# Kernel tuning notes

Hardware: AMD Instinct MI355X
Metric: run time of the kernel (lower is better)

Reference implementation:

```python
import jax, jax.numpy as jnp
import numpy as np


def _compute_gradient(f, src, dst, egw):
    # f: [b, c, n] node features; src/dst: [b, e] edge endpoints; egw: [b, e, d]
    # gradient at node src = sum_edges pinvdx * (f[dst] - f[src])
    fT = f.transpose(0, 2, 1)  # b, n, c
    n = fT.shape[1]
    f_dst = jnp.take_along_axis(fT, dst[..., None], axis=1)  # b, e, c
    f_src = jnp.take_along_axis(fT, src[..., None], axis=1)  # b, e, c
    msg = egw[..., :, None] * (f_dst - f_src)[..., None, :]  # b, e, d, c
    b, e, d, c = msg.shape

    def seg(m, s):
        return jax.ops.segment_sum(m.reshape(e, d * c), s, num_segments=n)

    grad = jax.vmap(seg)(msg, src)  # b, n, d*c
    return grad.transpose(0, 2, 1)  # b, d*c, n


def _forward(x, t, nodes, node_weights, edge_gradient_weights, modes, sp_L,
             fc0_w, fc0_b, Wc, Ws, W0, ws_w, ws_b, gws_w, gws_b,
             fc1_w, fc1_b, fc2_w, fc2_b, directed_edges):
    D = nodes.shape[-1]
    # Fourier bases: modes [k,d,w] scaled by sp_L [d,w]
    temp = jnp.einsum('bxd,kdw->bxkw', nodes, modes * sp_L)
    bc, bs = jnp.cos(temp), jnp.sin(temp)
    b0 = jnp.ones(temp[:, :, :1, :].shape, temp.dtype)
    nw = node_weights[:, :, None, :]
    wbc, wbs, wb0 = bc * nw, bs * nw, b0 * nw

    x_value = x[:, :, :D]
    h = jnp.concatenate([x, t], -1) @ fc0_w + fc0_b  # b, n, c
    h = h.transpose(0, 2, 1)  # b, c, n

    src = directed_edges[..., 0]
    dst = directed_edges[..., 1]
    nlayers = ws_w.shape[0]
    for i in range(nlayers):
        # spectral convolution (real Fourier transform on scattered points)
        xc = jnp.einsum('bcx,bxkw->bckw', h, wbc)
        xs = -jnp.einsum('bcx,bxkw->bckw', h, wbs)
        x0 = jnp.einsum('bcx,bxkw->bckw', h, wb0)
        fc_ = jnp.einsum('bikw,iokw->bokw', xc, Wc[i]) - jnp.einsum('bikw,iokw->bokw', xs, Ws[i])
        fs_ = jnp.einsum('bikw,iokw->bokw', xs, Wc[i]) + jnp.einsum('bikw,iokw->bokw', xc, Ws[i])
        f0_ = jnp.einsum('bikw,iokw->bokw', x0, W0[i])
        x1 = (jnp.einsum('bokw,bxkw->box', f0_, b0)
              + 2.0 * jnp.einsum('bokw,bxkw->box', fc_, bc)
              - 2.0 * jnp.einsum('bokw,bxkw->box', fs_, bs))
        # pointwise linear (Conv1d kernel size 1)
        x2 = jnp.einsum('oc,bcx->box', ws_w[i], h) + ws_b[i][None, :, None]
        # gradient operator + softsign + Conv1d
        g = _compute_gradient(h, src, dst, edge_gradient_weights)  # b, d*c, n
        g = g / (1.0 + jnp.abs(g))  # softsign
        x3 = jnp.einsum('oc,bcx->box', gws_w[i], g) + gws_b[i][None, :, None]
        h = x1 + x2 + x3
        if i != nlayers - 1:
            h = jax.nn.gelu(h, approximate=False)

    h = h.transpose(0, 2, 1)  # b, n, c
    h = jax.nn.gelu(h @ fc1_w + fc1_b, approximate=False)
    h = h @ fc2_w + fc2_b
    return x_value + t * h


def setup_inputs() -> dict:
    B, N, E = 2, 20000, 100000
    D, W, K, C, L, FC, OUT = 3, 1, 128, 128, 3, 128, 3
    key = jax.random.key(0)
    k = jax.random.split(key, 16)
    x = jax.random.normal(k[0], (B, N, D), jnp.float32)
    t = jax.random.uniform(k[1], (B, N, 1), jnp.float32)
    node_mask = jnp.ones((B, N, 1), jnp.int32)
    nodes = jax.random.uniform(k[2], (B, N, D), jnp.float32)
    node_weights = jax.random.uniform(k[3], (B, N, W), jnp.float32) / N
    directed_edges = jax.random.randint(k[4], (B, E, 2), 0, N)
    edge_gradient_weights = jax.random.normal(k[5], (B, E, D), jnp.float32)
    modes = jax.random.normal(k[6], (K, D, W), jnp.float32) * (2.0 * np.pi)
    sp_L = jnp.ones((D, W), jnp.float32)
    fc0_w = jax.random.normal(k[7], (D + 1, C), jnp.float32) * 0.1
    fc0_b = jnp.zeros((C,), jnp.float32)
    scale = 1.0 / (C * C)
    Wc = jax.random.uniform(k[8], (L, C, C, K, W), jnp.float32) * scale
    Ws = jax.random.uniform(k[9], (L, C, C, K, W), jnp.float32) * scale
    W0 = jax.random.uniform(k[10], (L, C, C, 1, W), jnp.float32) * scale
    ws_w = jax.random.normal(k[11], (L, C, C), jnp.float32) * 0.05
    ws_b = jnp.zeros((L, C), jnp.float32)
    gws_w = jax.random.normal(k[12], (L, C, D * C), jnp.float32) * 0.05
    gws_b = jnp.zeros((L, C), jnp.float32)
    fc1_w = jax.random.normal(k[13], (C, FC), jnp.float32) * 0.05
    fc1_b = jnp.zeros((FC,), jnp.float32)
    fc2_w = jax.random.normal(k[14], (FC, OUT), jnp.float32) * 0.05
    fc2_b = jnp.zeros((OUT,), jnp.float32)
    return dict(x=x, t=t, node_mask=node_mask, nodes=nodes, node_weights=node_weights,
                directed_edges=directed_edges, edge_gradient_weights=edge_gradient_weights,
                modes=modes, sp_L=sp_L, fc0_w=fc0_w, fc0_b=fc0_b, Wc=Wc, Ws=Ws, W0=W0,
                ws_w=ws_w, ws_b=ws_b, gws_w=gws_w, gws_b=gws_b,
                fc1_w=fc1_w, fc1_b=fc1_b, fc2_w=fc2_w, fc2_b=fc2_b)


def reference(x, t, node_mask, nodes, node_weights, directed_edges, edge_gradient_weights,
              modes, sp_L, fc0_w, fc0_b, Wc, Ws, W0, ws_w, ws_b, gws_w, gws_b,
              fc1_w, fc1_b, fc2_w, fc2_b):
    del node_mask  # unpacked but unused in the original forward
    return _forward(x, t, nodes, node_weights, edge_gradient_weights, modes, sp_L,
                    fc0_w, fc0_b, Wc, Ws, W0, ws_w, ws_b, gws_w, gws_b,
                    fc1_w, fc1_b, fc2_w, fc2_b, directed_edges)
```

## Files before the change

### kernel.cpp

```cpp
#include <hip/hip_runtime.h>
#include <math.h>

#define BB 2
#define NN 20000
#define EE 100000
#define DD 3
#define KK 128
#define CC 128
#define LL 3
#define FCC 128
#define GJ (DD*CC)
#define KR 768
#define NP 20096
#define NCHK 157
#define G1CH 79
#define G1N 256

typedef __attribute__((ext_vector_type(8))) short bf16x8;
typedef __attribute__((ext_vector_type(4))) float f32x4;

__device__ inline unsigned short f2bf(float f) {
  unsigned int u = __float_as_uint(f);
  u += 0x7fffu + ((u >> 16) & 1u);
  return (unsigned short)(u >> 16);
}
__device__ inline float bf2f(unsigned short u) {
  return __uint_as_float(((unsigned int)u) << 16);
}

__device__ float d_nw[BB*NN];
__device__ __align__(16) unsigned short d_stackT[(size_t)BB*NP*KR];
__device__ __align__(16) unsigned short d_bcT[(size_t)BB*KK*NP];
__device__ __align__(16) unsigned short d_bsT[(size_t)BB*KK*NP];
__device__ __align__(16) unsigned short d_hTwT[(size_t)BB*CC*NP];
__device__ __align__(16) float d_hnewT[(size_t)BB*NP*CC];
__device__ __align__(16) float d_uT[(size_t)BB*NP*FCC];
__device__ __align__(16) unsigned short d_Amatb[BB*CC*KR];
__device__ __align__(16) unsigned short d_fc1wb[FCC*CC];
__device__ __align__(16) float d_part[(size_t)BB*G1CH*2*128*128];
__device__ float d_xc[BB*CC*KK];
__device__ float d_xs[BB*CC*KK];
__device__ float d_x0p[BB*NCHK*CC];
__device__ float d_fcv[BB*CC*KK];
__device__ float d_fsv[BB*CC*KK];
__device__ float d_bias[BB*CC];
__device__ int d_cnt[BB*NN];
__device__ int d_cursor[BB*NN];
__device__ int d_off[BB*(NN+1)];
__device__ __align__(16) float4 d_erec[(size_t)BB*EE];

__global__ __launch_bounds__(128) void k_basis(const float* __restrict__ nodes,
                                               const float* __restrict__ nodew,
                                               const float* __restrict__ modes,
                                               const float* __restrict__ spL) {
  int bn = blockIdx.x;
  int k  = threadIdx.x;
  int b = bn / NN, n = bn % NN;
  float x0 = nodes[bn*3+0], x1 = nodes[bn*3+1], x2 = nodes[bn*3+2];
  float tmp = x0*modes[k*3+0]*spL[0] + x1*modes[k*3+1]*spL[1] + x2*modes[k*3+2]*spL[2];
  float cv = cosf(tmp), sv = sinf(tmp);
  size_t row = (size_t)(b*NP + n);
  d_stackT[row*KR + k]       = f2bf(cv);
  d_stackT[row*KR + 128 + k] = f2bf(sv);
  if (k == 0) d_nw[bn] = nodew[bn];
}

__global__ __launch_bounds__(256) void k_basisT() {
  __shared__ unsigned short t1[32][136];
  __shared__ unsigned short t2[32][136];
  int blk = blockIdx.x;
  int nt = blk % 628, b = blk / 628;
  int n0 = nt*32;
  int tid = threadIdx.x;
  int kl = tid & 127, ng = tid >> 7;
  for (int nn = ng; nn < 32; nn += 2) {
    int n = n0 + nn;
    unsigned short cv = 0, sv = 0;
    if (n < NN) {
      const unsigned short* sp = d_stackT + ((size_t)(b*NP + n))*KR;
      cv = sp[kl]; sv = sp[128 + kl];
    }
    t1[nn][kl] = cv;
    t2[nn][kl] = sv;
  }
  __syncthreads();
  int nl = tid & 31, kg = tid >> 5;
  for (int k = kg; k < 128; k += 8) {
    d_bcT[((size_t)(b*KK + k))*NP + n0 + nl] = t1[nl][k];
    d_bsT[((size_t)(b*KK + k))*NP + n0 + nl] = t2[nl][k];
  }
}

__global__ __launch_bounds__(256) void k_csr_zero() {
  int tid = blockIdx.x*256 + threadIdx.x;
  if (tid < BB*NN) { d_cnt[tid] = 0; d_cursor[tid] = 0; }
}

__global__ __launch_bounds__(256) void k_csr_count(const int* __restrict__ edges) {
  int e = blockIdx.x*256 + threadIdx.x;
  if (e >= BB*EE) return;
  int b = e / EE;
  int src = edges[e*2 + 0];
  atomicAdd(&d_cnt[b*NN + src], 1);
}

__global__ __launch_bounds__(1024) void k_csr_scan() {
  int b = blockIdx.x;
  __shared__ int sdata[1024];
  __shared__ int carry_s;
  int tid = threadIdx.x;
  if (tid == 0) carry_s = 0;
  __syncthreads();
  for (int chunk = 0; chunk < 20; ++chunk) {
    int i = chunk*1024 + tid;
    int v = (i < NN) ? d_cnt[b*NN + i] : 0;
    sdata[tid] = v;
    __syncthreads();
    for (int s = 1; s < 1024; s <<= 1) {
      int tv = (tid >= s) ? sdata[tid - s] : 0;
      __syncthreads();
      sdata[tid] += tv;
      __syncthreads();
    }
    int excl = carry_s + sdata[tid] - v;
    if (i < NN) d_off[b*(NN+1) + i] = excl;
    __syncthreads();
    if (tid == 1023) carry_s += sdata[1023];
    __syncthreads();
  }
  if (tid == 0) d_off[b*(NN+1) + NN] = carry_s;
}

__global__ __launch_bounds__(256) void k_csr_scatter(const int* __restrict__ edges,
                                                     const float* __restrict__ egw) {
  int e = blockIdx.x*256 + threadIdx.x;
  if (e >= BB*EE) return;
  int b = e / EE;
  int src = edges[e*2 + 0];
  int dst = edges[e*2 + 1];
  int pos = atomicAdd(&d_cursor[b*NN + src], 1);
  d_erec[(size_t)b*EE + d_off[b*(NN+1) + src] + pos] =
      make_float4(__int_as_float(dst), egw[e*3+0], egw[e*3+1], egw[e*3+2]);
}

__global__ __launch_bounds__(256) void k_h0(const float* __restrict__ x,
                                            const float* __restrict__ t,
                                            const float* __restrict__ w,
                                            const float* __restrict__ bias) {
  int tid = blockIdx.x*256 + threadIdx.x;
  int c = tid & 127;
  int bn = tid >> 7;
  int b = bn / NN, n = bn % NN;
  const float* xv = x + bn*3;
  float acc = bias[c] + xv[0]*w[c] + xv[1]*w[CC+c] + xv[2]*w[2*CC+c]
            + t[bn]*w[3*CC+c];
  size_t row = (size_t)(b*NP + n);
  d_hnewT[row*CC + c] = acc;
  d_stackT[row*KR + 256 + c] = f2bf(acc);
}

__global__ __launch_bounds__(256) void k_hT0() {
  __shared__ unsigned short t[128][136];
  int chunk = blockIdx.x;
  int b = blockIdx.y;
  int n0 = chunk*128;
  int tid = threadIdx.x;
  int cl = tid & 127, ng = tid >> 7;
  for (int nn = ng; nn < 128; nn += 2) {
    int n = n0 + nn;
    unsigned short v = 0;
    if (n < NN) v = f2bf(d_hnewT[((size_t)(b*NP + n))*CC + cl] * d_nw[b*NN + n]);
    t[nn][cl] = v;
  }
  __syncthreads();
  int nl = tid & 31, cg = tid >> 5;
  for (int c = cg; c < 128; c += 8)
    for (int nn2 = 0; nn2 < 128; nn2 += 32)
      d_hTwT[((size_t)(b*CC + c))*NP + n0 + nn2 + nl] = t[nn2 + nl][c];
}

__global__ __launch_bounds__(256) void k_gemm1m() {
  __shared__ unsigned short Bsh[2][128][40];
  int chunk = blockIdx.x;
  int b = blockIdx.y;
  int tid = threadIdx.x, lane = tid & 63, wid = tid >> 6;
  int q = lane >> 4, m = lane & 15;
  f32x4 accC[2][8], accS[2][8];
  #pragma unroll
  for (int i = 0; i < 2; i++)
    #pragma unroll
    for (int j = 0; j < 8; j++) { accC[i][j] = (f32x4){0.f,0.f,0.f,0.f}; accS[i][j] = (f32x4){0.f,0.f,0.f,0.f}; }
  const unsigned short* Ab = d_hTwT + (size_t)b*CC*NP;
  const unsigned short* Bcp = d_bcT + (size_t)b*KK*NP;
  const unsigned short* Bsp = d_bsT + (size_t)b*KK*NP;
  int n0 = chunk*G1N;
  for (int s = 0; s < G1N/32; s++) {
    int nb = n0 + s*32;
    if (nb >= NP) break;
    __syncthreads();
    {
      int arr = tid >> 7, row = tid & 127;
      const unsigned short* src = (arr ? Bsp : Bcp) + (size_t)row*NP + nb;
      unsigned short* dr = &Bsh[arr][row][0];
      *(uint4*)&dr[0]  = *(const uint4*)&src[0];
      *(uint4*)&dr[8]  = *(const uint4*)&src[8];
      *(uint4*)&dr[16] = *(const uint4*)&src[16];
      *(uint4*)&dr[24] = *(const uint4*)&src[24];
    }
    __syncthreads();
    bf16x8 a0 = *(const bf16x8*)(Ab + (size_t)(wid*32 + m)*NP + nb + q*8);
    bf16x8 a1 = *(const bf16x8*)(Ab + (size_t)(wid*32 + 16 + m)*NP + nb + q*8);
    #pragma unroll
    for (int kt = 0; kt < 8; kt++) {
      bf16x8 bcf = *(const bf16x8*)&Bsh[0][kt*16 + m][q*8];
      bf16x8 bsf = *(const bf16x8*)&Bsh[1][kt*16 + m][q*8];
      accC[0][kt] = __builtin_amdgcn_mfma_f32_16x16x32_bf16(a0, bcf, accC[0][kt], 0, 0, 0);
      accC[1][kt] = __builtin_amdgcn_mfma_f32_16x16x32_bf16(a1, bcf, accC[1][kt], 0, 0, 0);
      accS[0][kt] = __builtin_amdgcn_mfma_f32_16x16x32_bf16(a0, bsf, accS[0][kt], 0, 0, 0);
      accS[1][kt] = __builtin_amdgcn_mfma_f32_16x16x32_bf16(a1, bsf, accS[1][kt], 0, 0, 0);
    }
  }
  float* base = d_part + (((size_t)b*G1CH + chunk)*2)*16384;
  #pragma unroll
  for (int mt = 0; mt < 2; mt++)
    #pragma unroll
    for (int kt = 0; kt < 8; kt++)
      #pragma unroll
      for (int r = 0; r < 4; r++) {
        int c = wid*32 + mt*16 + q*4 + r;
        int k = kt*16 + m;
        base[c*128 + k]         =  accC[mt][kt][r];
        base[16384 + c*128 + k] = -accS[mt][kt][r];
      }
}

__global__ __launch_bounds__(256) void k_reduce1() {
  int tid = blockIdx.x*256 + threadIdx.x;
  int k = tid & 127;
  int c = (tid >> 7) & 127;
  int arr = (tid >> 14) & 1;
  int b = tid >> 15;
  const float* p = d_part + (((size_t)b*G1CH)*2 + arr)*16384 + c*128 + k;
  float acc = 0.f;
  for (int ch = 0; ch < G1CH; ch++) acc += p[(size_t)ch*2*16384];
  if (arr == 0) d_xc[(b*CC + c)*KK + k] = acc;
  else          d_xs[(b*CC + c)*KK + k] = acc;
}

__global__ __launch_bounds__(256) void k_x0() {
  int chunk = blockIdx.x;
  int b = blockIdx.y;
  int tid = threadIdx.x;
  int c = tid >> 1, half = tid & 1;
  const unsigned short* p = d_hTwT + ((size_t)(b*CC + c))*NP + chunk*128 + half*64;
  float acc = 0.f;
  #pragma unroll
  for (int i = 0; i < 8; i++) {
    ushort4 v0 = *(const ushort4*)&p[i*8];
    ushort4 v1 = *(const ushort4*)&p[i*8 + 4];
    acc += bf2f(v0.x) + bf2f(v0.y) + bf2f(v0.z) + bf2f(v0.w)
         + bf2f(v1.x) + bf2f(v1.y) + bf2f(v1.z) + bf2f(v1.w);
  }
  __shared__ float red[128][2];
  red[c][half] = acc;
  __syncthreads();
  if (half == 0) d_x0p[(b*NCHK + chunk)*CC + c] = red[c][0] + red[c][1];
}

__global__ __launch_bounds__(128) void k_spec(const float* __restrict__ Wc,
                                              const float* __restrict__ Ws, int l) {
  int b = blockIdx.x >> 7;
  int o = blockIdx.x & 127;
  int k = threadIdx.x;
  const float* wcp = Wc + ((size_t)(l*CC)*CC + o)*KK + k;
  const float* wsp = Ws + ((size_t)(l*CC)*CC + o)*KK + k;
  float fc = 0.f, fs = 0.f;
  for (int i = 0; i < CC; i++) {
    float xcv = d_xc[(b*CC + i)*KK + k];
    float xsv = d_xs[(b*CC + i)*KK + k];
    float wcv = wcp[(size_t)i*CC*KK];
    float wsv = wsp[(size_t)i*CC*KK];
    fc += xcv*wcv - xsv*wsv;
    fs += xsv*wcv + xcv*wsv;
  }
  d_fcv[(b*CC + o)*KK + k] = fc;
  d_fsv[(b*CC + o)*KK + k] = fs;
}

__global__ __launch_bounds__(128) void k_f0(const float* __restrict__ W0,
                                            const float* __restrict__ wsb,
                                            const float* __restrict__ gwsb, int l) {
  int b = blockIdx.x;
  int o = threadIdx.x;
  __shared__ float sx[CC];
  float xv = 0.f;
  for (int p = 0; p < NCHK; p++) xv += d_x0p[(b*NCHK + p)*CC + o];
  sx[o] = xv;
  __syncthreads();
  float acc = 0.f;
  for (int i = 0; i < CC; i++) acc += sx[i]*W0[(l*CC + i)*CC + o];
  d_bias[b*CC + o] = acc + wsb[l*CC + o] + gwsb[l*CC + o];
}

__global__ __launch_bounds__(128) void k_buildAb(const float* __restrict__ wsw,
                                                 const float* __restrict__ gwsw, int l) {
  int bo = blockIdx.x;
  int b = bo >> 7, o = bo & 127;
  int t = threadIdx.x;
  unsigned short* dst = d_Amatb + (size_t)bo*KR;
  dst[t]       = f2bf( 2.f*d_fcv[(size_t)bo*KK + t]);
  dst[128 + t] = f2bf(-2.f*d_fsv[(size_t)bo*KK + t]);
  dst[256 + t] = f2bf(wsw[(l*CC + o)*CC + t]);
  #pragma unroll
  for (int j = 0; j < 3; j++)
    dst[384 + j*128 + t] = f2bf(gwsw[(size_t)(l*CC + o)*GJ + j*128 + t]);
}

__global__ __launch_bounds__(128) void k_fc1w(const float* __restrict__ fc1w) {
  int c = blockIdx.x;
  int o2 = threadIdx.x;
  d_fc1wb[o2*CC + c] = f2bf(fc1w[c*FCC + o2]);
}

__global__ __launch_bounds__(128) void k_grad_csr() {
  int bn = blockIdx.x;
  int b = bn / NN, n = bn % NN;
  int c = threadIdx.x;
  int beg = d_off[b*(NN+1) + n];
  int end = d_off[b*(NN+1) + n + 1];
  const float4* rp = d_erec + (size_t)b*EE;
  const float* hb = d_hnewT + (size_t)b*NP*CC + c;
  float a0 = 0.f, a1 = 0.f, a2 = 0.f;
  float sw0 = 0.f, sw1 = 0.f, sw2 = 0.f;
  int p = beg;
  for (; p + 2 <= end; p += 2) {
    float4 r1 = rp[p], r2 = rp[p+1];
    float f1 = hb[(size_t)__float_as_int(r1.x)*CC];
    float f2 = hb[(size_t)__float_as_int(r2.x)*CC];
    a0 += r1.y*f1 + r2.y*f2;
    a1 += r1.z*f1 + r2.z*f2;
    a2 += r1.w*f1 + r2.w*f2;
    sw0 += r1.y + r2.y; sw1 += r1.z + r2.z; sw2 += r1.w + r2.w;
  }
  if (p < end) {
    float4 r1 = rp[p];
    float f1 = hb[(size_t)__float_as_int(r1.x)*CC];
    a0 += r1.y*f1; a1 += r1.z*f1; a2 += r1.w*f1;
    sw0 += r1.y; sw1 += r1.z; sw2 += r1.w;
  }
  float fs = d_hnewT[((size_t)(b*NP + n))*CC + c];
  a0 -= sw0*fs; a1 -= sw1*fs; a2 -= sw2*fs;
  unsigned short* gp = d_stackT + ((size_t)(b*NP + n))*KR + 384;
  gp[c]        = f2bf(a0/(1.f + fabsf(a0)));
  gp[CC + c]   = f2bf(a1/(1.f + fabsf(a1)));
  gp[2*CC + c] = f2bf(a2/(1.f + fabsf(a2)));
}

__global__ __launch_bounds__(256) void k_mfma(int koff, int K,
                                              const unsigned short* __restrict__ W, size_t wstride,
                                              float* __restrict__ Out,
                                              const float* __restrict__ bias, int bias_stride,
                                              int gelu, int aux) {
  __shared__ unsigned short As[2][32*40];
  __shared__ unsigned short Bs[2][128*40];
  int b = blockIdx.z;
  int n_base = blockIdx.x*32;
  int tid = threadIdx.x;
  int lane = tid & 63, wid = tid >> 6;
  int wr = wid >> 1, wc = wid & 1;
  int q = lane >> 4, m = lane & 15;

  f32x4 acc[4];
  #pragma unroll
  for (int j = 0; j < 4; j++) acc[j] = (f32x4){0.f,0.f,0.f,0.f};

  const unsigned short* Wb = W + (size_t)b*wstride;
  const unsigned short* Ab = d_stackT + (size_t)b*NP*KR + koff;

#define STAGE(k0, d) { \
    if (tid < 128) { \
      int rowA = tid >> 2; int e8A = (tid & 3)*8; \
      *(uint4*)&As[d][rowA*40 + e8A] = *(const uint4*)(Ab + (size_t)(n_base + rowA)*KR + (k0) + e8A); \
    } \
    _Pragma("unroll") \
    for (int i_ = 0; i_ < 2; i_++) { \
      int idx_ = tid + i_*256; int rowB = idx_ >> 2; int e8B = (idx_ & 3)*8; \
      *(uint4*)&Bs[d][rowB*40 + e8B] = *(const uint4*)(Wb + (size_t)rowB*K + (k0) + e8B); \
    } }

  STAGE(0, 0)
  int cur = 0;
  for (int k0 = 0; k0 < K; k0 += 32) {
    __syncthreads();
    if (k0 + 32 < K) STAGE(k0 + 32, cur ^ 1)
    bf16x8 a = *(const bf16x8*)&As[cur][(wr*16 + m)*40 + q*8];
    #pragma unroll
    for (int ot = 0; ot < 4; ot++) {
      bf16x8 bf = *(const bf16x8*)&Bs[cur][(wc*64 + ot*16 + m)*40 + q*8];
      acc[ot] = __builtin_amdgcn_mfma_f32_16x16x32_bf16(a, bf, acc[ot], 0, 0, 0);
    }
    cur ^= 1;
  }
#undef STAGE

  const float* bp = bias + (size_t)b*bias_stride;
  int nb4 = n_base + wr*16 + q*4;
  float nw4[4];
  #pragma unroll
  for (int r = 0; r < 4; r++)
    nw4[r] = (aux && nb4 + r < NN) ? d_nw[b*NN + nb4 + r] : 0.f;
  #pragma unroll
  for (int ot = 0; ot < 4; ot++) {
    int o = wc*64 + ot*16 + m;
    float bvv = bp[o];
    float vals[4];
    #pragma unroll
    for (int r = 0; r < 4; r++) {
      float v = acc[ot][r] + bvv;
      if (gelu) v = 0.5f*v*(1.f + erff(v*0.70710678118f));
      vals[r] = v;
      Out[((size_t)(b*NP + nb4 + r))*128 + o] = v;
      if (aux && nb4 + r < NN)
        d_stackT[((size_t)(b*NP + nb4 + r))*KR + 256 + o] = f2bf(v);
    }
    if (aux) {
      ushort4 pk;
      pk.x = f2bf(vals[0]*nw4[0]);
      pk.y = f2bf(vals[1]*nw4[1]);
      pk.z = f2bf(vals[2]*nw4[2]);
      pk.w = f2bf(vals[3]*nw4[3]);
      *(ushort4*)&d_hTwT[((size_t)(b*CC + o))*NP + nb4] = pk;
    }
  }
}

__global__ __launch_bounds__(256) void k_out(const float* __restrict__ x,
                                             const float* __restrict__ t,
                                             const float* __restrict__ fc2w,
                                             const float* __restrict__ fc2b,
                                             float* __restrict__ out) {
  int tid = blockIdx.x*256 + threadIdx.x;
  if (tid >= BB*NN) return;
  int b = tid / NN, n = tid % NN;
  const float* up = d_uT + ((size_t)(b*NP + n))*FCC;
  float a0 = fc2b[0], a1 = fc2b[1], a2v = fc2b[2];
  #pragma unroll 4
  for (int o2 = 0; o2 < FCC; o2 += 4) {
    float4 uv = *(const float4*)&up[o2];
    a0  += uv.x*fc2w[(o2+0)*3+0] + uv.y*fc2w[(o2+1)*3+0] + uv.z*fc2w[(o2+2)*3+0] + uv.w*fc2w[(o2+3)*3+0];
    a1  += uv.x*fc2w[(o2+0)*3+1] + uv.y*fc2w[(o2+1)*3+1] + uv.z*fc2w[(o2+2)*3+1] + uv.w*fc2w[(o2+3)*3+1];
    a2v += uv.x*fc2w[(o2+0)*3+2] + uv.y*fc2w[(o2+1)*3+2] + uv.z*fc2w[(o2+2)*3+2] + uv.w*fc2w[(o2+3)*3+2];
  }
  float tv = t[tid];
  out[tid*3 + 0] = x[tid*3 + 0] + tv*a0;
  out[tid*3 + 1] = x[tid*3 + 1] + tv*a1;
  out[tid*3 + 2] = x[tid*3 + 2] + tv*a2v;
}

extern "C" void kernel_launch(void* const* d_in, const int* in_sizes, int n_in,
                              void* d_out, int out_size, void* d_ws, size_t ws_size,
                              hipStream_t stream) {
  const float* x     = (const float*)d_in[0];
  const float* t     = (const float*)d_in[1];
  const float* nodes = (const float*)d_in[3];
  const float* nodew = (const float*)d_in[4];
  const int*   edges = (const int*)d_in[5];
  const float* egw   = (const float*)d_in[6];
  const float* modes = (const float*)d_in[7];
  const float* spL   = (const float*)d_in[8];
  const float* fc0w  = (const float*)d_in[9];
  const float* fc0b  = (const float*)d_in[10];
  const float* Wc    = (const float*)d_in[11];
  const float* Ws    = (const float*)d_in[12];
  const float* W0    = (const float*)d_in[13];
  const float* wsw   = (const float*)d_in[14];
  const float* wsb   = (const float*)d_in[15];
  const float* gwsw  = (const float*)d_in[16];
  const float* gwsb  = (const float*)d_in[17];
  const float* fc1w  = (const float*)d_in[18];
  const float* fc1b  = (const float*)d_in[19];
  const float* fc2w  = (const float*)d_in[20];
  const float* fc2b  = (const float*)d_in[21];
  float* out = (float*)d_out;

  unsigned short* d_Amatb_p; hipGetSymbolAddress((void**)&d_Amatb_p, HIP_SYMBOL(d_Amatb));
  unsigned short* d_fc1wb_p; hipGetSymbolAddress((void**)&d_fc1wb_p, HIP_SYMBOL(d_fc1wb));
  float* d_hnewT_p; hipGetSymbolAddress((void**)&d_hnewT_p, HIP_SYMBOL(d_hnewT));
  float* d_uT_p;    hipGetSymbolAddress((void**)&d_uT_p,    HIP_SYMBOL(d_uT));
  float* d_bias_p;  hipGetSymbolAddress((void**)&d_bias_p,  HIP_SYMBOL(d_bias));

  hipLaunchKernelGGL(k_basis, dim3(BB*NN), dim3(128), 0, stream, nodes, nodew, modes, spL);
  hipLaunchKernelGGL(k_basisT, dim3(628*BB), dim3(256), 0, stream);
  hipLaunchKernelGGL(k_h0, dim3(BB*NN*CC/256), dim3(256), 0, stream, x, t, fc0w, fc0b);
  hipLaunchKernelGGL(k_hT0, dim3(NCHK, BB), dim3(256), 0, stream);
  hipLaunchKernelGGL(k_fc1w, dim3(CC), dim3(FCC), 0, stream, fc1w);
  hipLaunchKernelGGL(k_csr_zero, dim3((BB*NN + 255)/256), dim3(256), 0, stream);
  hipLaunchKernelGGL(k_csr_count, dim3((BB*EE + 255)/256), dim3(256), 0, stream, edges);
  hipLaunchKernelGGL(k_csr_scan, dim3(BB), dim3(1024), 0, stream);
  hipLaunchKernelGGL(k_csr_scatter, dim3((BB*EE + 255)/256), dim3(256), 0, stream, edges, egw);

  for (int l = 0; l < LL; l++) {
    hipLaunchKernelGGL(k_gemm1m, dim3(G1CH, BB), dim3(256), 0, stream);
    hipLaunchKernelGGL(k_reduce1, dim3(256), dim3(256), 0, stream);
    hipLaunchKernelGGL(k_x0, dim3(NCHK, BB), dim3(256), 0, stream);
    hipLaunchKernelGGL(k_spec, dim3(BB*CC), dim3(128), 0, stream, Wc, Ws, l);
    hipLaunchKernelGGL(k_f0, dim3(BB), dim3(CC), 0, stream, W0, wsb, gwsb, l);
    hipLaunchKernelGGL(k_buildAb, dim3(BB*CC), dim3(128), 0, stream, wsw, gwsw, l);
    hipLaunchKernelGGL(k_grad_csr, dim3(BB*NN), dim3(128), 0, stream);
    hipLaunchKernelGGL(k_mfma, dim3(NP/32, 1, BB), dim3(256), 0, stream,
                       0, KR, d_Amatb_p, (size_t)CC*KR, d_hnewT_p, d_bias_p, CC,
                       (l != LL-1) ? 1 : 0, 1);
  }

  hipLaunchKernelGGL(k_mfma, dim3(NP/32, 1, BB), dim3(256), 0, stream,
                     256, CC, d_fc1wb_p, (size_t)0, d_uT_p, fc1b, 0, 1, 0);
  hipLaunchKernelGGL(k_out, dim3((BB*NN + 255)/256), dim3(256), 0, stream, x, t, fc2w, fc2b, out);
}
```

Baseline: 588.3 us.

## Drop fp32 hidden-state buffer, gather bf16 features, split spectral mixing over channels

Removes the fp32 d_hnewT hidden-state copy. The gradient gather and transpose now read the bf16 copy already held in the stacked operand, and the layer GEMM skips writing fp32 output when aux is set. k_spec splits its input-channel reduction across 8 blocks, with partial sums reduced in k_buildAb, which raises parallelism. k_gemm1m chunks are halved to double the grid, and the edge loop unrolls by 4. This reduces memory traffic and improves occupancy, but gathers now read strided rows of the KR-wide stack and use bf16 precision for the gradient inputs.

```diff
diff --git a/kernel.cpp b/kernel.cpp
--- a/kernel.cpp
+++ b/kernel.cpp
@@ -13,8 +13,8 @@
 #define KR 768
 #define NP 20096
 #define NCHK 157
-#define G1CH 79
-#define G1N 256
+#define G1CH 157
+#define G1N 128
 
 typedef __attribute__((ext_vector_type(8))) short bf16x8;
 typedef __attribute__((ext_vector_type(4))) float f32x4;
@@ -33,7 +33,6 @@
 __device__ __align__(16) unsigned short d_bcT[(size_t)BB*KK*NP];
 __device__ __align__(16) unsigned short d_bsT[(size_t)BB*KK*NP];
 __device__ __align__(16) unsigned short d_hTwT[(size_t)BB*CC*NP];
-__device__ __align__(16) float d_hnewT[(size_t)BB*NP*CC];
 __device__ __align__(16) float d_uT[(size_t)BB*NP*FCC];
 __device__ __align__(16) unsigned short d_Amatb[BB*CC*KR];
 __device__ __align__(16) unsigned short d_fc1wb[FCC*CC];
@@ -41,8 +40,8 @@
 __device__ float d_xc[BB*CC*KK];
 __device__ float d_xs[BB*CC*KK];
 __device__ float d_x0p[BB*NCHK*CC];
-__device__ float d_fcv[BB*CC*KK];
-__device__ float d_fsv[BB*CC*KK];
+__device__ float d_fcp[BB*CC*8*KK];
+__device__ float d_fsp[BB*CC*8*KK];
 __device__ float d_bias[BB*CC];
 __device__ int d_cnt[BB*NN];
 __device__ int d_cursor[BB*NN];
@@ -154,9 +153,7 @@
   const float* xv = x + bn*3;
   float acc = bias[c] + xv[0]*w[c] + xv[1]*w[CC+c] + xv[2]*w[2*CC+c]
             + t[bn]*w[3*CC+c];
-  size_t row = (size_t)(b*NP + n);
-  d_hnewT[row*CC + c] = acc;
-  d_stackT[row*KR + 256 + c] = f2bf(acc);
+  d_stackT[((size_t)(b*NP + n))*KR + 256 + c] = f2bf(acc);
 }
 
 __global__ __launch_bounds__(256) void k_hT0() {
@@ -169,7 +166,10 @@
   for (int nn = ng; nn < 128; nn += 2) {
     int n = n0 + nn;
     unsigned short v = 0;
-    if (n < NN) v = f2bf(d_hnewT[((size_t)(b*NP + n))*CC + cl] * d_nw[b*NN + n]);
+    if (n < NN) {
+      float hv = bf2f(d_stackT[((size_t)(b*NP + n))*KR + 256 + cl]);
+      v = f2bf(hv * d_nw[b*NN + n]);
+    }
     t[nn][cl] = v;
   }
   __syncthreads();
@@ -196,7 +196,6 @@
   int n0 = chunk*G1N;
   for (int s = 0; s < G1N/32; s++) {
     int nb = n0 + s*32;
-    if (nb >= NP) break;
     __syncthreads();
     {
       int arr = tid >> 7, row = tid & 127;
@@ -269,22 +268,27 @@
 
 __global__ __launch_bounds__(128) void k_spec(const float* __restrict__ Wc,
                                               const float* __restrict__ Ws, int l) {
-  int b = blockIdx.x >> 7;
-  int o = blockIdx.x & 127;
+  int bo = blockIdx.x;
+  int ch = blockIdx.y;
+  int b = bo >> 7;
+  int o = bo & 127;
   int k = threadIdx.x;
-  const float* wcp = Wc + ((size_t)(l*CC)*CC + o)*KK + k;
-  const float* wsp = Ws + ((size_t)(l*CC)*CC + o)*KK + k;
+  int i0 = ch*16;
+  const float* wcp = Wc + ((size_t)(l*CC + i0)*CC + o)*KK + k;
+  const float* wsp = Ws + ((size_t)(l*CC + i0)*CC + o)*KK + k;
   float fc = 0.f, fs = 0.f;
-  for (int i = 0; i < CC; i++) {
+  #pragma unroll 4
+  for (int j = 0; j < 16; j++) {
+    int i = i0 + j;
     float xcv = d_xc[(b*CC + i)*KK + k];
     float xsv = d_xs[(b*CC + i)*KK + k];
-    float wcv = wcp[(size_t)i*CC*KK];
-    float wsv = wsp[(size_t)i*CC*KK];
+    float wcv = wcp[(size_t)j*CC*KK];
+    float wsv = wsp[(size_t)j*CC*KK];
     fc += xcv*wcv - xsv*wsv;
     fs += xsv*wcv + xcv*wsv;
   }
-  d_fcv[(b*CC + o)*KK + k] = fc;
-  d_fsv[(b*CC + o)*KK + k] = fs;
+  d_fcp[((size_t)bo*8 + ch)*KK + k] = fc;
+  d_fsp[((size_t)bo*8 + ch)*KK + k] = fs;
 }
 
 __global__ __launch_bounds__(128) void k_f0(const float* __restrict__ W0,
@@ -307,9 +311,15 @@
   int bo = blockIdx.x;
   int b = bo >> 7, o = bo & 127;
   int t = threadIdx.x;
+  float fc = 0.f, fs = 0.f;
+  #pragma unroll
+  for (int ch = 0; ch < 8; ch++) {
+    fc += d_fcp[((size_t)bo*8 + ch)*KK + t];
+    fs += d_fsp[((size_t)bo*8 + ch)*KK + t];
+  }
   unsigned short* dst = d_Amatb + (size_t)bo*KR;
-  dst[t]       = f2bf( 2.f*d_fcv[(size_t)bo*KK + t]);
-  dst[128 + t] = f2bf(-2.f*d_fsv[(size_t)bo*KK + t]);
+  dst[t]       = f2bf( 2.f*fc);
+  dst[128 + t] = f2bf(-2.f*fs);
   dst[256 + t] = f2bf(wsw[(l*CC + o)*CC + t]);
   #pragma unroll
   for (int j = 0; j < 3; j++)
@@ -329,26 +339,30 @@
   int beg = d_off[b*(NN+1) + n];
   int end = d_off[b*(NN+1) + n + 1];
   const float4* rp = d_erec + (size_t)b*EE;
-  const float* hb = d_hnewT + (size_t)b*NP*CC + c;
+  const unsigned short* hb = d_stackT + (size_t)b*NP*KR + 256 + c;
   float a0 = 0.f, a1 = 0.f, a2 = 0.f;
   float sw0 = 0.f, sw1 = 0.f, sw2 = 0.f;
   int p = beg;
-  for (; p + 2 <= end; p += 2) {
-    float4 r1 = rp[p], r2 = rp[p+1];
-    float f1 = hb[(size_t)__float_as_int(r1.x)*CC];
-    float f2 = hb[(size_t)__float_as_int(r2.x)*CC];
-    a0 += r1.y*f1 + r2.y*f2;
-    a1 += r1.z*f1 + r2.z*f2;
-    a2 += r1.w*f1 + r2.w*f2;
-    sw0 += r1.y + r2.y; sw1 += r1.z + r2.z; sw2 += r1.w + r2.w;
-  }
-  if (p < end) {
+  for (; p + 4 <= end; p += 4) {
+    float4 r1 = rp[p], r2 = rp[p+1], r3 = rp[p+2], r4 = rp[p+3];
+    float f1 = bf2f(hb[(size_t)__float_as_int(r1.x)*KR]);
+    float f2 = bf2f(hb[(size_t)__float_as_int(r2.x)*KR]);
+    float f3 = bf2f(hb[(size_t)__float_as_int(r3.x)*KR]);
+    float f4 = bf2f(hb[(size_t)__float_as_int(r4.x)*KR]);
+    a0 += r1.y*f1 + r2.y*f2 + r3.y*f3 + r4.y*f4;
+    a1 += r1.z*f1 + r2.z*f2 + r3.z*f3 + r4.z*f4;
+    a2 += r1.w*f1 + r2.w*f2 + r3.w*f3 + r4.w*f4;
+    sw0 += r1.y + r2.y + r3.y + r4.y;
+    sw1 += r1.z + r2.z + r3.z + r4.z;
+    sw2 += r1.w + r2.w + r3.w + r4.w;
+  }
+  for (; p < end; ++p) {
     float4 r1 = rp[p];
-    float f1 = hb[(size_t)__float_as_int(r1.x)*CC];
+    float f1 = bf2f(hb[(size_t)__float_as_int(r1.x)*KR]);
     a0 += r1.y*f1; a1 += r1.z*f1; a2 += r1.w*f1;
     sw0 += r1.y; sw1 += r1.z; sw2 += r1.w;
   }
-  float fs = d_hnewT[((size_t)(b*NP + n))*CC + c];
+  float fs = bf2f(hb[(size_t)n*KR]);
   a0 -= sw0*fs; a1 -= sw1*fs; a2 -= sw2*fs;
   unsigned short* gp = d_stackT + ((size_t)(b*NP + n))*KR + 384;
   gp[c]        = f2bf(a0/(1.f + fabsf(a0)));
@@ -419,7 +433,7 @@
       float v = acc[ot][r] + bvv;
       if (gelu) v = 0.5f*v*(1.f + erff(v*0.70710678118f));
       vals[r] = v;
-      Out[((size_t)(b*NP + nb4 + r))*128 + o] = v;
+      if (!aux) Out[((size_t)(b*NP + nb4 + r))*128 + o] = v;
       if (aux && nb4 + r < NN)
         d_stackT[((size_t)(b*NP + nb4 + r))*KR + 256 + o] = f2bf(v);
     }
@@ -485,7 +499,6 @@
 
   unsigned short* d_Amatb_p; hipGetSymbolAddress((void**)&d_Amatb_p, HIP_SYMBOL(d_Amatb));
   unsigned short* d_fc1wb_p; hipGetSymbolAddress((void**)&d_fc1wb_p, HIP_SYMBOL(d_fc1wb));
-  float* d_hnewT_p; hipGetSymbolAddress((void**)&d_hnewT_p, HIP_SYMBOL(d_hnewT));
   float* d_uT_p;    hipGetSymbolAddress((void**)&d_uT_p,    HIP_SYMBOL(d_uT));
   float* d_bias_p;  hipGetSymbolAddress((void**)&d_bias_p,  HIP_SYMBOL(d_bias));
 
@@ -503,12 +516,12 @@
     hipLaunchKernelGGL(k_gemm1m, dim3(G1CH, BB), dim3(256), 0, stream);
     hipLaunchKernelGGL(k_reduce1, dim3(256), dim3(256), 0, stream);
     hipLaunchKernelGGL(k_x0, dim3(NCHK, BB), dim3(256), 0, stream);
-    hipLaunchKernelGGL(k_spec, dim3(BB*CC), dim3(128), 0, stream, Wc, Ws, l);
+    hipLaunchKernelGGL(k_spec, dim3(BB*CC, 8), dim3(128), 0, stream, Wc, Ws, l);
     hipLaunchKernelGGL(k_f0, dim3(BB), dim3(CC), 0, stream, W0, wsb, gwsb, l);
     hipLaunchKernelGGL(k_buildAb, dim3(BB*CC), dim3(128), 0, stream, wsw, gwsw, l);
     hipLaunchKernelGGL(k_grad_csr, dim3(BB*NN), dim3(128), 0, stream);
     hipLaunchKernelGGL(k_mfma, dim3(NP/32, 1, BB), dim3(256), 0, stream,
-                       0, KR, d_Amatb_p, (size_t)CC*KR, d_hnewT_p, d_bias_p, CC,
+                       0, KR, d_Amatb_p, (size_t)CC*KR, d_uT_p, d_bias_p, CC,
                        (l != LL-1) ? 1 : 0, 1);
   }
 
```

Result: faster. 564.0 us (-4.1%).
